# Kernel tuning notes

Measured on AMD Instinct MI355X. Metric: run time of the kernel, lower is better.

## Reference

```python
import jax, jax.numpy as jnp
import numpy as np
from jax.scipy.special import logsumexp

V, E, H, T, L = 50000, 256, 128, 64, 4096
D = int(np.log2(L))          # leaves live at heap level D
N = 2 * L - 1                # total nodes in perfect binary tree (heap indexing)


def _postorder(n_total):
    order = []
    def rec(i):
        if 2 * i + 1 < n_total:
            rec(2 * i + 1)
            rec(2 * i + 2)
        order.append(i)
    rec(0)
    return np.array(order, dtype=np.int32)

POST = _postorder(N)


def setup_inputs() -> dict:
    key = jax.random.key(0)
    ks = jax.random.split(key, 8)
    s = lambda k, shape, fan: (jax.random.normal(k, shape, jnp.float32) / np.sqrt(fan).astype(np.float32))
    return {
        "tokens": jax.random.randint(ks[0], (L,), 0, V),
        "emb": s(ks[1], (V, E), E),
        "W_ih": s(ks[2], (4 * H, E), E),
        "W_hh": s(ks[3], (4 * H, H), H),
        "b_ih": jnp.zeros((4 * H,), jnp.float32),
        "b_hh": jnp.zeros((4 * H,), jnp.float32),
        "W_p2h": s(ks[4], (H, 2 * H), 2 * H),
        "b_p2h": jnp.zeros((H,), jnp.float32),
        "W_uni": s(ks[5], (T, H), H),
        "b_uni": jnp.zeros((T,), jnp.float32),
        "W_edge": s(ks[6], (T * T, 2 * H), 2 * H),
        "b_edge": jnp.zeros((T * T,), jnp.float32),
    }


def reference(tokens, emb, W_ih, W_hh, b_ih, b_hh, W_p2h, b_p2h,
              W_uni, b_uni, W_edge, b_edge):
    # ---- Encoder: embedding + single-layer LSTM over the leaf sequence ----
    x = emb[tokens]                                   # [L, E]
    def step(carry, xt):
        h, c = carry
        g = W_ih @ xt + b_ih + W_hh @ h + b_hh        # torch gate order i,f,g,o
        i, f, gg, o = jnp.split(g, 4)
        c = jax.nn.sigmoid(f) * c + jax.nn.sigmoid(i) * jnp.tanh(gg)
        h = jax.nn.sigmoid(o) * jnp.tanh(c)
        return (h, c), h
    z = jnp.zeros((H,), x.dtype)
    _, leaf_h = jax.lax.scan(step, (z, z), x)         # [L, H]

    # ---- build_node_to_hidden: bottom-up per-level pair fusion ----
    hidden = jnp.zeros((N, H), x.dtype).at[L - 1:].set(leaf_h)
    for d in range(D - 1, -1, -1):
        idx = jnp.arange(2 ** d - 1, 2 ** (d + 1) - 1)
        pair = jnp.concatenate([hidden[2 * idx + 1], hidden[2 * idx + 2]], axis=1)
        hidden = hidden.at[idx].set(pair @ W_p2h.T + b_p2h)

    # ---- build_factors (batched over all nodes / edges) ----
    unary = hidden @ W_uni.T + b_uni                  # [N, T]
    child = jnp.arange(1, N)
    parent = (child - 1) // 2
    pair = jnp.concatenate([hidden[parent], hidden[child]], axis=1)
    edge_fac = (pair @ W_edge.T + b_edge).reshape(N - 1, T, T)  # edge (parent,child), idx = child-1

    # ---- upward pass (level-synchronous, bottom-up) ----
    v2f = unary                                       # node -> top factor message
    f2p = jnp.zeros((N, T), x.dtype)                  # factor -> parent message, indexed by child
    for d in range(D, -1, -1):
        idx = jnp.arange(2 ** d - 1, 2 ** (d + 1) - 1)
        if d < D:  # internal nodes: add both children's factor->node messages
            v2f = v2f.at[idx].add(f2p[2 * idx + 1] + f2p[2 * idx + 2])
        if d > 0:  # message through top edge factor to the parent
            f2p = f2p.at[idx].set(
                logsumexp(edge_fac[idx - 1] + v2f[idx][:, None, :], axis=2))

    # ---- downward pass (level-synchronous, top-down) ----
    f2n = jnp.zeros((N, T), x.dtype)                  # top-factor -> node message; root gets none
    for d in range(1, D + 1):
        idx = jnp.arange(2 ** d - 1, 2 ** (d + 1) - 1)
        par = (idx - 1) // 2
        sib = jnp.where(idx % 2 == 1, idx + 1, idx - 1)
        p2f = unary[par] + f2n[par] + f2p[sib]        # parent's messages, excluding this child's
        f2n = f2n.at[idx].set(
            logsumexp(edge_fac[idx - 1] + p2f[:, :, None], axis=1))

    beliefs = v2f + f2n                               # sum of all incoming messages, [N, T]
    return beliefs[POST]                              # stacked in postorder, like the original
```

## Files before the change

### kernel.cpp

```cpp
#include <hip/hip_runtime.h>
#include <hip/hip_bf16.h>

typedef __hip_bfloat16 bf16;
typedef float fx2 __attribute__((ext_vector_type(2)));

#define NL 4096
#define NH 128
#define NE 256
#define NT 64
#define NNODE 8191
#define NDEPTH 12

#define OF_WIH   0
#define OF_WHH   131072
#define OF_BIH   196608
#define OF_BHH   197120
#define OF_WP2H  197632
#define OF_BP2H  230400
#define OF_WUNI  230528
#define OF_BUNI  238720
#define OF_WEDGE 238784
#define OF_BEDGE 1287360
#define WF_TOTAL 1291456

__device__ __forceinline__ float b2f(bf16 x) { return __bfloat162float(x); }

__global__ void detect_kernel(const void* __restrict__ wedge_raw, int* __restrict__ flag) {
  __shared__ int cnt_sh[256];
  const unsigned short* p = (const unsigned short*)wedge_raw;
  int c = 0;
  for (int i = threadIdx.x; i < 32768; i += 256) {
    float v = __uint_as_float(((unsigned)p[2 * i]) << 16);
    if (fabsf(v) > 4.f) c++;
  }
  cnt_sh[threadIdx.x] = c;
  __syncthreads();
  for (int s = 128; s > 0; s >>= 1) {
    if (threadIdx.x < s) cnt_sh[threadIdx.x] += cnt_sh[threadIdx.x + s];
    __syncthreads();
  }
  if (threadIdx.x == 0) *flag = cnt_sh[0];
}

__global__ void convert_kernel(const void* s0, const void* s1, const void* s2, const void* s3,
                               const void* s4, const void* s5, const void* s6, const void* s7,
                               const void* s8, const void* s9,
                               const int* __restrict__ flag, float* __restrict__ wf) {
  int i = blockIdx.x * 256 + threadIdx.x;
  if (i >= WF_TOTAL) return;
  const void* src; int local;
  if      (i < OF_WHH)   { src = s0; local = i; }
  else if (i < OF_BIH)   { src = s1; local = i - OF_WHH; }
  else if (i < OF_BHH)   { src = s2; local = i - OF_BIH; }
  else if (i < OF_WP2H)  { src = s3; local = i - OF_BHH; }
  else if (i < OF_BP2H)  { src = s4; local = i - OF_WP2H; }
  else if (i < OF_WUNI)  { src = s5; local = i - OF_BP2H; }
  else if (i < OF_BUNI)  { src = s6; local = i - OF_WUNI; }
  else if (i < OF_WEDGE) { src = s7; local = i - OF_BUNI; }
  else if (i < OF_BEDGE) { src = s8; local = i - OF_WEDGE; }
  else                   { src = s9; local = i - OF_BEDGE; }
  bool isf32 = (*flag) > 100;
  wf[i] = isf32 ? ((const float*)src)[local] : b2f(((const bf16*)src)[local]);
}

__global__ __launch_bounds__(512) void g1_kernel(const int* __restrict__ tokens,
                                                 const void* __restrict__ emb_raw,
                                                 const int* __restrict__ flag,
                                                 const float* __restrict__ wf,
                                                 float* __restrict__ G1) {
  __shared__ __attribute__((aligned(16))) float xs[8 * NE];
  const bool isf32 = (*flag) > 100;
  const int t0 = blockIdx.x * 8;
  for (int q = threadIdx.x; q < 8 * NE; q += 512) {
    int tok = q >> 8, e = q & 255;
    size_t off = (size_t)tokens[t0 + tok] * NE + e;
    xs[q] = isf32 ? ((const float*)emb_raw)[off] : b2f(((const bf16*)emb_raw)[off]);
  }
  __syncthreads();
  const int r = threadIdx.x;
  const float bias = wf[OF_BIH + r] + wf[OF_BHH + r];
  float acc[8];
#pragma unroll
  for (int k = 0; k < 8; ++k) acc[k] = bias;
  const float4* W4 = (const float4*)(wf + OF_WIH + (size_t)r * NE);
#pragma unroll 8
  for (int j = 0; j < 64; ++j) {
    float4 wv = W4[j];
#pragma unroll
    for (int tok = 0; tok < 8; ++tok) {
      float4 xv = ((const float4*)(xs + tok * NE))[j];
      acc[tok] += wv.x * xv.x + wv.y * xv.y + wv.z * xv.z + wv.w * xv.w;
    }
  }
#pragma unroll
  for (int tok = 0; tok < 8; ++tok) G1[(size_t)(t0 + tok) * 512 + r] = acc[tok];
}

__global__ __launch_bounds__(512, 2) void lstm_kernel(const float* __restrict__ wf,
                                                      const float* __restrict__ G1,
                                                      float* __restrict__ hidden) {
  const int r = threadIdx.x;
  __shared__ __attribute__((aligned(16))) float h_sh[NH];
  __shared__ float g_sh[512];
  fx2 w[64];
  const float4* W4 = (const float4*)(wf + OF_WHH + (size_t)r * NH);
#pragma unroll
  for (int j = 0; j < 32; ++j) {
    float4 v = W4[j];
    fx2 p0, p1; p0.x = v.x; p0.y = v.y; p1.x = v.z; p1.y = v.w;
    w[2 * j] = p0; w[2 * j + 1] = p1;
  }
#pragma unroll
  for (int j = 0; j < 64; ++j) asm volatile("" : "+v"(w[j]));
  float c = 0.f;
  if (r < NH) h_sh[r] = 0.f;
  __syncthreads();
  float gnext = G1[r];
  for (int t = 0; t < NL; ++t) {
    float gcur = gnext;
    if (t + 1 < NL) gnext = G1[(size_t)(t + 1) * 512 + r];
    fx2 a0 = {0.f, 0.f}, a1 = {0.f, 0.f}, a2 = {0.f, 0.f}, a3 = {0.f, 0.f};
    const float4* h4 = (const float4*)h_sh;
#pragma unroll
    for (int j = 0; j < 16; ++j) {
      float4 h0 = h4[2 * j], h1 = h4[2 * j + 1];
      fx2 e0, e1, e2, e3;
      e0.x = h0.x; e0.y = h0.y; e1.x = h0.z; e1.y = h0.w;
      e2.x = h1.x; e2.y = h1.y; e3.x = h1.z; e3.y = h1.w;
      a0 += w[4 * j + 0] * e0;
      a1 += w[4 * j + 1] * e1;
      a2 += w[4 * j + 2] * e2;
      a3 += w[4 * j + 3] * e3;
    }
    g_sh[r] = gcur + (a0.x + a0.y) + (a1.x + a1.y) + (a2.x + a2.y) + (a3.x + a3.y);
    __syncthreads();
    if (r < NH) {
      float iv = g_sh[r], fv = g_sh[r + 128], gv = g_sh[r + 256], ov = g_sh[r + 384];
      float si = 1.f / (1.f + __expf(-iv));
      float sf = 1.f / (1.f + __expf(-fv));
      float tg = 1.f - 2.f / (__expf(2.f * gv) + 1.f);
      float so = 1.f / (1.f + __expf(-ov));
      c = sf * c + si * tg;
      float hh = so * (1.f - 2.f / (__expf(2.f * c) + 1.f));
      h_sh[r] = hh;
      hidden[(size_t)(NL - 1 + t) * NH + r] = hh;
    }
    __syncthreads();
  }
}

__global__ void p2h_kernel(const float* __restrict__ wf, float* __restrict__ hidden, int base) {
  int node = base + blockIdx.x;
  int j = threadIdx.x;
  __shared__ __attribute__((aligned(16))) float pr[2 * NH];
  const float* hl = hidden + (size_t)(2 * node + 1) * NH;
  pr[j] = hl[j];
  pr[j + NH] = hl[j + NH];
  __syncthreads();
  float acc = wf[OF_BP2H + j];
  const float4* W4 = (const float4*)(wf + OF_WP2H + (size_t)j * 2 * NH);
  const float4* p4 = (const float4*)pr;
#pragma unroll 16
  for (int q = 0; q < 64; ++q) {
    float4 u = W4[q], x = p4[q];
    acc += u.x * x.x + u.y * x.y + u.z * x.z + u.w * x.w;
  }
  hidden[(size_t)node * NH + j] = acc;
}

__global__ void unary_kernel(const float* __restrict__ wf, const float* __restrict__ hidden,
                             float* __restrict__ unary, float* __restrict__ f2n) {
  int node = blockIdx.x;
  int ct = threadIdx.x;
  __shared__ __attribute__((aligned(16))) float hs[NH];
  hs[ct] = hidden[(size_t)node * NH + ct];
  hs[ct + 64] = hidden[(size_t)node * NH + 64 + ct];
  __syncthreads();
  float acc = wf[OF_BUNI + ct];
  const float4* W4 = (const float4*)(wf + OF_WUNI + (size_t)ct * NH);
  const float4* h4 = (const float4*)hs;
#pragma unroll
  for (int q = 0; q < 32; ++q) {
    float4 u = W4[q], x = h4[q];
    acc += u.x * x.x + u.y * x.y + u.z * x.z + u.w * x.w;
  }
  unary[(size_t)node * NT + ct] = acc;
  if (node == 0) f2n[ct] = 0.f;
}

__global__ __launch_bounds__(256) void edge_kernel(const float* __restrict__ hidden,
                                                   const float* __restrict__ wf,
                                                   float* __restrict__ edge) {
  __shared__ __attribute__((aligned(16))) float As[32][132];
  __shared__ __attribute__((aligned(16))) float Bs[32][132];
  const int tid = threadIdx.x;
  const int nb = blockIdx.x;
  const int mb = blockIdx.y;
  const int tm = tid >> 4, tn = tid & 15;
  float acc[8][8];
#pragma unroll
  for (int i = 0; i < 8; ++i)
#pragma unroll
    for (int j = 0; j < 8; ++j) acc[i][j] = 0.f;
  const int sr = tid >> 1;
  const int sq = tid & 1;
  for (int ch = 0; ch < 8; ++ch) {
    {
      int gm = mb * 128 + sr;
      const float* srcA = (ch < 4) ? hidden + (size_t)(gm >> 1) * NH + ch * 32
                                   : hidden + (size_t)(gm + 1) * NH + (ch - 4) * 32;
      bool ok = (gm < NNODE - 1);
#pragma unroll
      for (int i = 0; i < 4; ++i) {
        int kk = sq * 16 + i * 4;
        float4 v = ok ? *(const float4*)(srcA + kk) : make_float4(0.f, 0.f, 0.f, 0.f);
        As[kk + 0][sr] = v.x; As[kk + 1][sr] = v.y; As[kk + 2][sr] = v.z; As[kk + 3][sr] = v.w;
      }
    }
    {
      int gn = nb * 128 + sr;
      const float* srcB = wf + OF_WEDGE + (size_t)gn * NE + ch * 32;
#pragma unroll
      for (int i = 0; i < 4; ++i) {
        int kk = sq * 16 + i * 4;
        float4 v = *(const float4*)(srcB + kk);
        Bs[kk + 0][sr] = v.x; Bs[kk + 1][sr] = v.y; Bs[kk + 2][sr] = v.z; Bs[kk + 3][sr] = v.w;
      }
    }
    __syncthreads();
#pragma unroll 8
    for (int kk = 0; kk < 32; ++kk) {
      float a[8], b[8];
      *(float4*)(a)     = *(const float4*)&As[kk][tm * 4];
      *(float4*)(a + 4) = *(const float4*)&As[kk][64 + tm * 4];
      *(float4*)(b)     = *(const float4*)&Bs[kk][tn * 4];
      *(float4*)(b + 4) = *(const float4*)&Bs[kk][64 + tn * 4];
#pragma unroll
      for (int i = 0; i < 8; ++i)
#pragma unroll
        for (int j = 0; j < 8; ++j) acc[i][j] += a[i] * b[j];
    }
    __syncthreads();
  }
  float bias[8];
#pragma unroll
  for (int j = 0; j < 8; ++j)
    bias[j] = wf[OF_BEDGE + nb * 128 + (j >> 2) * 64 + tn * 4 + (j & 3)];
#pragma unroll
  for (int i = 0; i < 8; ++i) {
    int gm = mb * 128 + (i >> 2) * 64 + tm * 4 + (i & 3);
    if (gm < NNODE - 1) {
      float* row = edge + (size_t)gm * 4096 + nb * 128;
      float4 o0, o1;
      o0.x = acc[i][0] + bias[0]; o0.y = acc[i][1] + bias[1];
      o0.z = acc[i][2] + bias[2]; o0.w = acc[i][3] + bias[3];
      o1.x = acc[i][4] + bias[4]; o1.y = acc[i][5] + bias[5];
      o1.z = acc[i][6] + bias[6]; o1.w = acc[i][7] + bias[7];
      *(float4*)(row + tn * 4) = o0;
      *(float4*)(row + 64 + tn * 4) = o1;
    }
  }
}

__global__ void up_kernel(const float* __restrict__ unary, const float* __restrict__ edge,
                          float* __restrict__ v2f, float* __restrict__ f2p,
                          int base, int depth) {
  int node = base + blockIdx.x;
  int tid = threadIdx.x;
  __shared__ __attribute__((aligned(16))) float vs[NT];
  float vv = unary[(size_t)node * NT + tid];
  if (depth < NDEPTH)
    vv += f2p[(size_t)(2 * node + 1) * NT + tid] + f2p[(size_t)(2 * node + 2) * NT + tid];
  v2f[(size_t)node * NT + tid] = vv;
  vs[tid] = vv;
  __syncthreads();
  if (depth == 0) return;
  const float4* E4 = (const float4*)(edge + (size_t)(node - 1) * 4096 + tid * 64);
  const float4* v4 = (const float4*)vs;
  float x[NT];
#pragma unroll
  for (int q = 0; q < 16; ++q) {
    float4 e = E4[q], vq = v4[q];
    x[4 * q + 0] = e.x + vq.x; x[4 * q + 1] = e.y + vq.y;
    x[4 * q + 2] = e.z + vq.z; x[4 * q + 3] = e.w + vq.w;
  }
  float m = x[0];
#pragma unroll
  for (int i = 1; i < NT; ++i) m = fmaxf(m, x[i]);
  float s = 0.f;
#pragma unroll
  for (int i = 0; i < NT; ++i) s += __expf(x[i] - m);
  f2p[(size_t)node * NT + tid] = m + __logf(s);
}

__global__ void down_kernel(const float* __restrict__ unary, const float* __restrict__ edge,
                            const float* __restrict__ f2p, float* __restrict__ f2n,
                            int base) {
  int node = base + blockIdx.x;
  int tid = threadIdx.x;
  int par = (node - 1) >> 1;
  int sib = (node & 1) ? node + 1 : node - 1;
  __shared__ __attribute__((aligned(16))) float us[NT];
  us[tid] = unary[(size_t)par * NT + tid] + f2n[(size_t)par * NT + tid] +
            f2p[(size_t)sib * NT + tid];
  __syncthreads();
  float uu[NT];
  const float4* u4 = (const float4*)us;
#pragma unroll
  for (int q = 0; q < 16; ++q) {
    float4 t4 = u4[q];
    uu[4 * q] = t4.x; uu[4 * q + 1] = t4.y; uu[4 * q + 2] = t4.z; uu[4 * q + 3] = t4.w;
  }
  const float* E = edge + (size_t)(node - 1) * 4096 + tid;
  float x[NT];
#pragma unroll
  for (int p = 0; p < NT; ++p) x[p] = E[(size_t)p * 64] + uu[p];
  float m = x[0];
#pragma unroll
  for (int i = 1; i < NT; ++i) m = fmaxf(m, x[i]);
  float s = 0.f;
#pragma unroll
  for (int i = 0; i < NT; ++i) s += __expf(x[i] - m);
  f2n[(size_t)node * NT + tid] = m + __logf(s);
}

__global__ void final_kernel(const float* __restrict__ v2f, const float* __restrict__ f2n,
                             const int* __restrict__ flag, void* __restrict__ out) {
  int node = blockIdx.x;
  int tid = threadIdx.x;
  unsigned v = (unsigned)node + 1u;
  int d = 31 - __clz((int)v);
  int b0 = 0, S = NNODE;
  for (int b = d - 1; b >= 0; --b) {
    int sz = (S - 1) >> 1;
    if ((v >> b) & 1) b0 += sz;
    S = sz;
  }
  int pos = b0 + S - 1;
  float val = v2f[(size_t)node * NT + tid] + f2n[(size_t)node * NT + tid];
  if ((*flag) > 100) ((float*)out)[(size_t)pos * NT + tid] = val;
  else               ((bf16*)out)[(size_t)pos * NT + tid] = __float2bfloat16(val);
}

extern "C" void kernel_launch(void* const* d_in, const int* in_sizes, int n_in,
                              void* d_out, int out_size, void* d_ws, size_t ws_size,
                              hipStream_t stream) {
  (void)in_sizes; (void)n_in; (void)out_size; (void)ws_size;
  const int* tokens = (const int*)d_in[0];

  float* ws     = (float*)d_ws;
  int*   flag   = (int*)ws;
  float* wf     = ws + 16;
  float* hidden = wf + WF_TOTAL;
  float* G1     = hidden + (size_t)NNODE * NH;
  float* unary  = G1 + (size_t)NL * 512;
  float* v2f    = unary + (size_t)NNODE * NT;
  float* f2p    = v2f + (size_t)NNODE * NT;
  float* f2n    = f2p + (size_t)NNODE * NT;
  float* edge   = f2n + (size_t)NNODE * NT;

  detect_kernel<<<1, 256, 0, stream>>>(d_in[10], flag);
  convert_kernel<<<(WF_TOTAL + 255) / 256, 256, 0, stream>>>(
      d_in[2], d_in[3], d_in[4], d_in[5], d_in[6], d_in[7],
      d_in[8], d_in[9], d_in[10], d_in[11], flag, wf);
  g1_kernel<<<NL / 8, 512, 0, stream>>>(tokens, d_in[1], flag, wf, G1);
  lstm_kernel<<<1, 512, 0, stream>>>(wf, G1, hidden);
  for (int d = NDEPTH - 1; d >= 0; --d)
    p2h_kernel<<<1 << d, 128, 0, stream>>>(wf, hidden, (1 << d) - 1);
  unary_kernel<<<NNODE, 64, 0, stream>>>(wf, hidden, unary, f2n);
  edge_kernel<<<dim3(32, 64), 256, 0, stream>>>(hidden, wf, edge);
  for (int d = NDEPTH; d >= 0; --d)
    up_kernel<<<1 << d, 64, 0, stream>>>(unary, edge, v2f, f2p, (1 << d) - 1, d);
  for (int d = 1; d <= NDEPTH; ++d)
    down_kernel<<<1 << d, 64, 0, stream>>>(unary, edge, f2p, f2n, (1 << d) - 1);
  final_kernel<<<NNODE, 64, 0, stream>>>(v2f, f2n, flag, d_out);
}
```

Before: 4.059 ms.

## Restructure LSTM recurrence: 256 threads each computing four gates over half of h

The LSTM kernel now uses 256 threads instead of 512. Each thread holds W_hh rows for all four gates of one hidden unit, restricted to half of the hidden dimension (128 fx2 registers). Partial sums are exchanged through shared memory, and the gate nonlinearity reads the four gates directly without a 512-wide g_sh scatter. The G1 precompute is written in an interleaved gate layout so each hidden unit loads its four gate inputs as one float4. The aim is fewer wavefronts per serial step and cheaper gate gathering, in exchange for much higher register pressure and a longer dot-product chain per thread.

```diff
diff --git a/kernel.cpp b/kernel.cpp
--- a/kernel.cpp
+++ b/kernel.cpp
@@ -92,58 +92,76 @@
       acc[tok] += wv.x * xv.x + wv.y * xv.y + wv.z * xv.z + wv.w * xv.w;
     }
   }
-#pragma unroll
-  for (int tok = 0; tok < 8; ++tok) G1[(size_t)(t0 + tok) * 512 + r] = acc[tok];
-}
-
-__global__ __launch_bounds__(512, 2) void lstm_kernel(const float* __restrict__ wf,
+  const int gi = (r & 127) * 4 + (r >> 7);
+#pragma unroll
+  for (int tok = 0; tok < 8; ++tok) G1[(size_t)(t0 + tok) * 512 + gi] = acc[tok];
+}
+
+__global__ __launch_bounds__(256, 1) void lstm_kernel(const float* __restrict__ wf,
                                                       const float* __restrict__ G1,
                                                       float* __restrict__ hidden) {
-  const int r = threadIdx.x;
+  const int tid = threadIdx.x;
+  const int j   = tid & 127;
+  const int kh  = tid >> 7;
   __shared__ __attribute__((aligned(16))) float h_sh[NH];
-  __shared__ float g_sh[512];
-  fx2 w[64];
-  const float4* W4 = (const float4*)(wf + OF_WHH + (size_t)r * NH);
-#pragma unroll
-  for (int j = 0; j < 32; ++j) {
-    float4 v = W4[j];
-    fx2 p0, p1; p0.x = v.x; p0.y = v.y; p1.x = v.z; p1.y = v.w;
-    w[2 * j] = p0; w[2 * j + 1] = p1;
-  }
-#pragma unroll
-  for (int j = 0; j < 64; ++j) asm volatile("" : "+v"(w[j]));
+  __shared__ __attribute__((aligned(16))) float part_sh[256][4];
+
+  fx2 w[4][32];
+#pragma unroll
+  for (int g = 0; g < 4; ++g) {
+    const float4* W4 = (const float4*)(wf + OF_WHH + (size_t)(j + 128 * g) * NH + 64 * kh);
+#pragma unroll
+    for (int q = 0; q < 16; ++q) {
+      float4 v = W4[q];
+      w[g][2 * q].x     = v.x; w[g][2 * q].y     = v.y;
+      w[g][2 * q + 1].x = v.z; w[g][2 * q + 1].y = v.w;
+    }
+  }
+#pragma unroll
+  for (int g = 0; g < 4; ++g)
+#pragma unroll
+    for (int q = 0; q < 32; ++q) asm volatile("" : "+v"(w[g][q]));
+
   float c = 0.f;
-  if (r < NH) h_sh[r] = 0.f;
-  __syncthreads();
-  float gnext = G1[r];
+  if (tid < NH) h_sh[tid] = 0.f;
+  __syncthreads();
+  float4 gnext = make_float4(0.f, 0.f, 0.f, 0.f);
+  if (kh == 0) gnext = *(const float4*)(G1 + (size_t)0 * 512 + j * 4);
   for (int t = 0; t < NL; ++t) {
-    float gcur = gnext;
-    if (t + 1 < NL) gnext = G1[(size_t)(t + 1) * 512 + r];
+    float4 gcur = gnext;
+    if (kh == 0 && t + 1 < NL)
+      gnext = *(const float4*)(G1 + (size_t)(t + 1) * 512 + j * 4);
     fx2 a0 = {0.f, 0.f}, a1 = {0.f, 0.f}, a2 = {0.f, 0.f}, a3 = {0.f, 0.f};
-    const float4* h4 = (const float4*)h_sh;
-#pragma unroll
-    for (int j = 0; j < 16; ++j) {
-      float4 h0 = h4[2 * j], h1 = h4[2 * j + 1];
-      fx2 e0, e1, e2, e3;
-      e0.x = h0.x; e0.y = h0.y; e1.x = h0.z; e1.y = h0.w;
-      e2.x = h1.x; e2.y = h1.y; e3.x = h1.z; e3.y = h1.w;
-      a0 += w[4 * j + 0] * e0;
-      a1 += w[4 * j + 1] * e1;
-      a2 += w[4 * j + 2] * e2;
-      a3 += w[4 * j + 3] * e3;
-    }
-    g_sh[r] = gcur + (a0.x + a0.y) + (a1.x + a1.y) + (a2.x + a2.y) + (a3.x + a3.y);
-    __syncthreads();
-    if (r < NH) {
-      float iv = g_sh[r], fv = g_sh[r + 128], gv = g_sh[r + 256], ov = g_sh[r + 384];
+    const float4* h4 = (const float4*)(h_sh + (kh << 6));
+#pragma unroll
+    for (int q = 0; q < 16; ++q) {
+      float4 hv = h4[q];
+      fx2 e0, e1;
+      e0.x = hv.x; e0.y = hv.y; e1.x = hv.z; e1.y = hv.w;
+      a0 += w[0][2 * q] * e0; a0 += w[0][2 * q + 1] * e1;
+      a1 += w[1][2 * q] * e0; a1 += w[1][2 * q + 1] * e1;
+      a2 += w[2][2 * q] * e0; a2 += w[2][2 * q + 1] * e1;
+      a3 += w[3][2 * q] * e0; a3 += w[3][2 * q + 1] * e1;
+    }
+    float4 pv;
+    pv.x = a0.x + a0.y; pv.y = a1.x + a1.y;
+    pv.z = a2.x + a2.y; pv.w = a3.x + a3.y;
+    *(float4*)part_sh[tid] = pv;
+    __syncthreads();
+    if (kh == 0) {
+      float4 po = *(const float4*)part_sh[tid + 128];
+      float iv = pv.x + po.x + gcur.x;
+      float fv = pv.y + po.y + gcur.y;
+      float gv = pv.z + po.z + gcur.z;
+      float ov = pv.w + po.w + gcur.w;
       float si = 1.f / (1.f + __expf(-iv));
       float sf = 1.f / (1.f + __expf(-fv));
       float tg = 1.f - 2.f / (__expf(2.f * gv) + 1.f);
       float so = 1.f / (1.f + __expf(-ov));
       c = sf * c + si * tg;
       float hh = so * (1.f - 2.f / (__expf(2.f * c) + 1.f));
-      h_sh[r] = hh;
-      hidden[(size_t)(NL - 1 + t) * NH + r] = hh;
+      h_sh[j] = hh;
+      hidden[(size_t)(NL - 1 + t) * NH + j] = hh;
     }
     __syncthreads();
   }
@@ -364,7 +382,7 @@
       d_in[2], d_in[3], d_in[4], d_in[5], d_in[6], d_in[7],
       d_in[8], d_in[9], d_in[10], d_in[11], flag, wf);
   g1_kernel<<<NL / 8, 512, 0, stream>>>(tokens, d_in[1], flag, wf, G1);
-  lstm_kernel<<<1, 512, 0, stream>>>(wf, G1, hidden);
+  lstm_kernel<<<1, 256, 0, stream>>>(wf, G1, hidden);
   for (int d = NDEPTH - 1; d >= 0; --d)
     p2h_kernel<<<1 << d, 128, 0, stream>>>(wf, hidden, (1 << d) - 1);
   unary_kernel<<<NNODE, 64, 0, stream>>>(wf, hidden, unary, f2n);
```

Result: slower. 5.153 ms (+27.0%).
